# Performance work log

Hardware: AMD Instinct MI355X
Metric: run time of the kernel (lower is better)

## Reference

```python
import jax, jax.numpy as jnp
import numpy as np

B, C, H, W = 8, 256, 64, 64
CQK = C // 8  # query/key channels = 32


def setup_inputs() -> dict:
    key = jax.random.key(0)
    ks = jax.random.split(key, 9)
    s_in = 1.0 / np.sqrt(C)  # conv2d default init scale (kernel_size=1)
    x = jax.random.normal(ks[0], (B, C, H, W), dtype=jnp.float32)
    Wq = jax.random.uniform(ks[1], (CQK, C), jnp.float32, -s_in, s_in)
    bq = jax.random.uniform(ks[2], (CQK,), jnp.float32, -s_in, s_in)
    Wk = jax.random.uniform(ks[3], (CQK, C), jnp.float32, -s_in, s_in)
    bk = jax.random.uniform(ks[4], (CQK,), jnp.float32, -s_in, s_in)
    Wv = jax.random.uniform(ks[5], (C, C), jnp.float32, -s_in, s_in)
    bv = jax.random.uniform(ks[6], (C,), jnp.float32, -s_in, s_in)
    Wf = jax.random.uniform(ks[7], (C, C), jnp.float32, -s_in, s_in)
    bf = jax.random.uniform(ks[8], (C,), jnp.float32, -s_in, s_in)
    return {"x": x, "Wq": Wq, "bq": bq, "Wk": Wk, "bk": bk,
            "Wv": Wv, "bv": bv, "Wf": Wf, "bf": bf}


def reference(x, Wq, bq, Wk, bk, Wv, bv, Wf, bf):
    b, c, h, w = x.shape
    n = h * w
    xf = x.reshape(b, c, n)  # [B, C, N]  (1x1 conv == channel matmul)
    q = jnp.einsum('oc,bcn->bon', Wq, xf) + bq[None, :, None]  # [B, C/8, N]
    k = jnp.einsum('oc,bcn->bon', Wk, xf) + bk[None, :, None]  # [B, C/8, N]
    v = jnp.einsum('oc,bcn->bon', Wv, xf) + bv[None, :, None]  # [B, C, N]
    # energy[b,i,j] = sum_c q[b,c,i] * k[b,c,j]; no scaling (matches source)
    energy = jnp.einsum('bci,bcj->bij', q, k)  # [B, N, N]
    attn = jax.nn.softmax(energy, axis=-1)
    # out[b,c,i] = sum_j v[b,c,j] * attn[b,i,j]
    out = jnp.einsum('bcj,bij->bci', v, attn)  # [B, C, N]
    out = jnp.einsum('oc,bcn->bon', Wf, out) + bf[None, :, None]
    return out.reshape(b, c, h, w)
```

## Files before the change

### kernel.cpp

```cpp
#include <hip/hip_runtime.h>
#include <hip/hip_bf16.h>

#define BATCH 8
#define CCH   256
#define NPOS  4096
#define CQK   32

typedef __attribute__((ext_vector_type(8))) short short8;
typedef __attribute__((ext_vector_type(4))) float f32x4;

__device__ inline unsigned short f2b(float f) {
    __hip_bfloat16 h = __float2bfloat16(f);
    return *reinterpret_cast<unsigned short*>(&h);
}

__device__ inline size_t qk_addr(int b, int n, int c) {
    return ((((size_t)b * 256 + (n >> 4)) * 4 + (c >> 3)) * 16 + (n & 15)) * 8 + (c & 7);
}
__device__ inline size_t v_addr(int b, int c, int j) {
    return (((((size_t)b * 128 + (j >> 5)) * 16 + (c >> 4)) * 4 + ((j >> 3) & 3)) * 16 + (c & 15)) * 8 + (j & 7);
}
__device__ inline size_t wsw_addr(int og, int c, int ol) {
    return ((size_t)(og * 8 + (c >> 5))) * 512 + (((c >> 3) & 3) * 16 + ol) * 8 + (c & 7);
}

__global__ __launch_bounds__(256, 4)
void prep_w_kernel(const float* __restrict__ Wq, const float* __restrict__ Wk,
                   const float* __restrict__ Wv, const float* __restrict__ Wf,
                   unsigned short* __restrict__ wsw)
{
    const int og = blockIdx.x;
    const int t  = threadIdx.x;
    const float* src; int orow;
    if (og < 2)       { src = Wq; orow = og * 16; }
    else if (og < 4)  { src = Wk; orow = (og - 2) * 16; }
    else if (og < 20) { src = Wv; orow = (og - 4) * 16; }
    else              { src = Wf; orow = (og - 20) * 16; }
    #pragma unroll
    for (int e = 0; e < 16; ++e) {
        int idx = t + e * 256;
        int ol = idx >> 8, c = idx & 255;
        wsw[wsw_addr(og, c, ol)] = f2b(src[(orow + ol) * 256 + c]);
    }
}

__global__ __launch_bounds__(256, 2)
void qkv_kernel(const float* __restrict__ x,
                const unsigned short* __restrict__ wsw,
                const float* __restrict__ bq, const float* __restrict__ bk,
                const float* __restrict__ bv,
                unsigned short* __restrict__ qb, unsigned short* __restrict__ kb,
                unsigned short* __restrict__ vb)
{
    __shared__ __align__(16) unsigned short xfrag[4][8][512];

    const int nt   = blockIdx.x;
    const int b    = blockIdx.y;
    const int t    = threadIdx.x;
    const int w    = t >> 6;
    const int lane = t & 63;
    const int q    = lane >> 4;
    const int ln   = lane & 15;
    const int lofs = (q * 16 + ln) * 8;

    {
        const float* xb = x + ((size_t)b * 256) * 4096 + (nt * 64 + w * 16 + ln);
        #pragma unroll
        for (int kk = 0; kk < 8; ++kk) {
            short8 s;
            #pragma unroll
            for (int j = 0; j < 8; ++j)
                ((unsigned short*)&s)[j] = f2b(xb[(size_t)(kk * 32 + q * 8 + j) * 4096]);
            *(short8*)&xfrag[w][kk][lane * 8] = s;
        }
    }
    __syncthreads();

    short8 wqk[8];
    #pragma unroll
    for (int kk = 0; kk < 8; ++kk)
        wqk[kk] = *(const short8*)(wsw + (size_t)(w * 8 + kk) * 512 + lofs);
    const float* bias = (w < 2) ? bq : bk;
    const int cb16 = (w & 1) * 16;
    const float b0 = bias[cb16 + q * 4 + 0];
    const float b1 = bias[cb16 + q * 4 + 1];
    const float b2 = bias[cb16 + q * 4 + 2];
    const float b3 = bias[cb16 + q * 4 + 3];
    unsigned short* dst = (w < 2) ? qb : kb;

    #pragma unroll
    for (int it = 0; it < 4; ++it) {
        short8 xf[8];
        #pragma unroll
        for (int kk = 0; kk < 8; ++kk)
            xf[kk] = *(const short8*)&xfrag[it][kk][lane * 8];

        {
            f32x4 acc = {b0, b1, b2, b3};
            #pragma unroll
            for (int kk = 0; kk < 8; ++kk)
                acc = __builtin_amdgcn_mfma_f32_16x16x32_bf16(wqk[kk], xf[kk], acc, 0, 0, 0);
            ushort4 s = {f2b(acc[0]), f2b(acc[1]), f2b(acc[2]), f2b(acc[3])};
            *(ushort4*)(dst + qk_addr(b, nt * 64 + it * 16 + ln, cb16 + q * 4)) = s;
        }

        #pragma unroll
        for (int oq = 0; oq < 4; ++oq) {
            const int c  = w * 64 + oq * 16 + ln;
            const float bb = bv[c];
            f32x4 acc = {bb, bb, bb, bb};
            const int og = 4 + w * 4 + oq;
            #pragma unroll
            for (int kk = 0; kk < 8; ++kk) {
                short8 bfr = *(const short8*)(wsw + (size_t)(og * 8 + kk) * 512 + lofs);
                acc = __builtin_amdgcn_mfma_f32_16x16x32_bf16(xf[kk], bfr, acc, 0, 0, 0);
            }
            ushort4 s = {f2b(acc[0]), f2b(acc[1]), f2b(acc[2]), f2b(acc[3])};
            *(ushort4*)(vb + v_addr(b, c, nt * 64 + it * 16 + q * 4)) = s;
        }
    }
}

__global__ __launch_bounds__(256, 2)
void attn_kernel(const unsigned short* __restrict__ qb,
                 const unsigned short* __restrict__ kb,
                 const unsigned short* __restrict__ vb,
                 const unsigned short* __restrict__ wsw,
                 const float* __restrict__ bfb, float* __restrict__ out)
{
    __shared__ __align__(16) unsigned short shbuf[64 * 264];
    __shared__ float lred[64];

    const int bid  = blockIdx.x;
    const int b    = bid & 7;
    const int i0   = (bid >> 3) * 64;
    const int t    = threadIdx.x;
    const int w    = t >> 6;
    const int lane = t & 63;
    const int quad = lane >> 4;
    const int ln   = lane & 15;

    const int ibase = i0 + w * 16;
    const int lofs  = (quad * 16 + ln) * 8;

    const short8 qfrag = *(const short8*)(qb + (((size_t)b * 256 + (ibase >> 4)) * 512) + lofs);

    f32x4 acc[4][4];
    #pragma unroll
    for (int it = 0; it < 4; ++it)
        #pragma unroll
        for (int cc = 0; cc < 4; ++cc) acc[it][cc] = (f32x4){0.f, 0.f, 0.f, 0.f};
    float accl[4] = {0.f, 0.f, 0.f, 0.f};

    const unsigned short* kbase = kb + (size_t)b * 256 * 512;
    const unsigned short* vbase = vb + (size_t)b * 128 * 8192;

    short8 kf[4], vf[4][2];
    #pragma unroll
    for (int jc = 0; jc < 4; ++jc)
        kf[jc] = *(const short8*)(kbase + (size_t)jc * 512 + lofs);
    #pragma unroll
    for (int cc = 0; cc < 4; ++cc) {
        vf[cc][0] = *(const short8*)(vbase + (w * 4 + cc) * 512 + lofs);
        vf[cc][1] = *(const short8*)(vbase + 8192 + (w * 4 + cc) * 512 + lofs);
    }

    int pb = 0;
    for (int j0 = 0; j0 < 4096; j0 += 64, pb ^= 1) {
        const int jn = (j0 + 64) & 4095;
        short8 kf_n[4], vf_n[4][2];
        #pragma unroll
        for (int jc = 0; jc < 4; ++jc)
            kf_n[jc] = *(const short8*)(kbase + ((size_t)((jn >> 4) + jc) * 512) + lofs);
        const unsigned short* vt_n = vbase + (size_t)(jn >> 5) * 8192;
        #pragma unroll
        for (int cc = 0; cc < 4; ++cc) {
            vf_n[cc][0] = *(const short8*)(vt_n + (w * 4 + cc) * 512 + lofs);
            vf_n[cc][1] = *(const short8*)(vt_n + 8192 + (w * 4 + cc) * 512 + lofs);
        }
        f32x4 s[4];
        #pragma unroll
        for (int jc = 0; jc < 4; ++jc)
            s[jc] = __builtin_amdgcn_mfma_f32_16x16x32_bf16(qfrag, kf[jc],
                     (f32x4){0.f, 0.f, 0.f, 0.f}, 0, 0, 0);
        #pragma unroll
        for (int jc = 0; jc < 4; ++jc) {
            #pragma unroll
            for (int r = 0; r < 4; ++r) {
                float p = __expf(s[jc][r]);
                accl[r] += p;
                shbuf[((size_t)(pb * 64 + w * 16 + quad * 4 + r)) * 72 + jc * 16 + ln] = f2b(p);
            }
        }
        __syncthreads();
        #pragma unroll
        for (int it = 0; it < 4; ++it) {
            const short8 pf0 = *(const short8*)&shbuf[((size_t)(pb * 64 + it * 16 + ln)) * 72 + quad * 8];
            const short8 pf1 = *(const short8*)&shbuf[((size_t)(pb * 64 + it * 16 + ln)) * 72 + 32 + quad * 8];
            #pragma unroll
            for (int cc = 0; cc < 4; ++cc) {
                acc[it][cc] = __builtin_amdgcn_mfma_f32_16x16x32_bf16(pf0, vf[cc][0], acc[it][cc], 0, 0, 0);
                acc[it][cc] = __builtin_amdgcn_mfma_f32_16x16x32_bf16(pf1, vf[cc][1], acc[it][cc], 0, 0, 0);
            }
        }
        #pragma unroll
        for (int jc = 0; jc < 4; ++jc) kf[jc] = kf_n[jc];
        #pragma unroll
        for (int cc = 0; cc < 4; ++cc) {
            vf[cc][0] = vf_n[cc][0];
            vf[cc][1] = vf_n[cc][1];
        }
    }

    #pragma unroll
    for (int r = 0; r < 4; ++r) {
        float v = accl[r];
        v += __shfl_xor(v, 1, 16);
        v += __shfl_xor(v, 2, 16);
        v += __shfl_xor(v, 4, 16);
        v += __shfl_xor(v, 8, 16);
        if (ln == 0) lred[w * 16 + quad * 4 + r] = v;
    }
    __syncthreads();

    #pragma unroll
    for (int it = 0; it < 4; ++it) {
        float linv[4];
        #pragma unroll
        for (int r = 0; r < 4; ++r) linv[r] = 1.f / lred[it * 16 + quad * 4 + r];
        #pragma unroll
        for (int cc = 0; cc < 4; ++cc) {
            const int c = w * 64 + cc * 16 + ln;
            #pragma unroll
            for (int r = 0; r < 4; ++r)
                shbuf[((size_t)(it * 16 + quad * 4 + r)) * 264 + c] = f2b(acc[it][cc][r] * linv[r]);
        }
    }
    __syncthreads();

    #pragma unroll
    for (int it = 0; it < 4; ++it) {
        short8 af[8];
        #pragma unroll
        for (int kk = 0; kk < 8; ++kk)
            af[kk] = *(const short8*)&shbuf[((size_t)(it * 16 + ln)) * 264 + kk * 32 + quad * 8];
        #pragma unroll
        for (int oq = 0; oq < 4; ++oq) {
            const int o  = w * 64 + oq * 16 + ln;
            const int og = 20 + w * 4 + oq;
            f32x4 pa = {0.f, 0.f, 0.f, 0.f};
            #pragma unroll
            for (int kk = 0; kk < 8; ++kk) {
                short8 bfr = *(const short8*)(wsw + (size_t)(og * 8 + kk) * 512 + lofs);
                pa = __builtin_amdgcn_mfma_f32_16x16x32_bf16(af[kk], bfr, pa, 0, 0, 0);
            }
            const float bias = bfb[o];
            float4 s = {pa[0] + bias, pa[1] + bias, pa[2] + bias, pa[3] + bias};
            *(float4*)(out + (size_t)(b * 256 + o) * 4096 + i0 + it * 16 + quad * 4) = s;
        }
    }
}

extern "C" void kernel_launch(void* const* d_in, const int* in_sizes, int n_in,
                              void* d_out, int out_size, void* d_ws, size_t ws_size,
                              hipStream_t stream)
{
    const float* x  = (const float*)d_in[0];
    const float* Wq = (const float*)d_in[1];
    const float* bq = (const float*)d_in[2];
    const float* Wk = (const float*)d_in[3];
    const float* bk = (const float*)d_in[4];
    const float* Wv = (const float*)d_in[5];
    const float* bv = (const float*)d_in[6];
    const float* Wf = (const float*)d_in[7];
    const float* bf = (const float*)d_in[8];
    float* out = (float*)d_out;

    unsigned short* qb  = (unsigned short*)d_ws;
    unsigned short* kb  = qb + (size_t)BATCH * NPOS * CQK;
    unsigned short* vb  = kb + (size_t)BATCH * NPOS * CQK;
    unsigned short* wsw = vb + (size_t)BATCH * CCH * NPOS;

    prep_w_kernel<<<36, 256, 0, stream>>>(Wq, Wk, Wv, Wf, wsw);
    qkv_kernel<<<dim3(64, 8), 256, 0, stream>>>(x, wsw, bq, bk, bv, qb, kb, vb);
    attn_kernel<<<512, 256, 0, stream>>>(qb, kb, vb, wsw, bf, out);
}
```

Before: 210.3 us.

## Coalesce x loads in QKV, widen to 512 threads, transpose score MFMA with swizzled LDS

The QKV kernel now reads x with float4 loads along the position axis into a padded row-major LDS tile. It runs 512 threads, so two groups of four waves each cover half of the position sub-tiles. The attention kernel swaps the MFMA operands so each lane holds four consecutive key scores for one query row. It writes them as a single 8-byte XOR-swizzled LDS store and reduces the row sum with two cross-quad shuffles instead of four per-row shuffle chains. These changes target uncoalesced strided global loads, scalar LDS stores, bank conflicts and shuffle overhead, at the cost of more LDS per QKV block and more complex addressing.

```diff
diff --git a/kernel.cpp b/kernel.cpp
--- a/kernel.cpp
+++ b/kernel.cpp
@@ -44,7 +44,7 @@
     }
 }
 
-__global__ __launch_bounds__(256, 2)
+__global__ __launch_bounds__(512, 2)
 void qkv_kernel(const float* __restrict__ x,
                 const unsigned short* __restrict__ wsw,
                 const float* __restrict__ bq, const float* __restrict__ bk,
@@ -52,7 +52,7 @@
                 unsigned short* __restrict__ qb, unsigned short* __restrict__ kb,
                 unsigned short* __restrict__ vb)
 {
-    __shared__ __align__(16) unsigned short xfrag[4][8][512];
+    __shared__ __align__(16) unsigned short xl[64 * 280];
 
     const int nt   = blockIdx.x;
     const int b    = blockIdx.y;
@@ -62,16 +62,21 @@
     const int q    = lane >> 4;
     const int ln   = lane & 15;
     const int lofs = (q * 16 + ln) * 8;
+    const int wq   = w & 3;
+    const int ith  = w >> 2;
 
     {
-        const float* xb = x + ((size_t)b * 256) * 4096 + (nt * 64 + w * 16 + ln);
-        #pragma unroll
-        for (int kk = 0; kk < 8; ++kk) {
-            short8 s;
-            #pragma unroll
-            for (int j = 0; j < 8; ++j)
-                ((unsigned short*)&s)[j] = f2b(xb[(size_t)(kk * 32 + q * 8 + j) * 4096]);
-            *(short8*)&xfrag[w][kk][lane * 8] = s;
+        const int c  = t & 255;
+        const int nb = (t >> 8) * 4;
+        const float* xb = x + ((size_t)(b * 256 + c)) * 4096 + nt * 64;
+        #pragma unroll
+        for (int e = 0; e < 8; ++e) {
+            const int n = nb + e * 8;
+            float4 v = *(const float4*)(xb + n);
+            xl[(n + 0) * 280 + c] = f2b(v.x);
+            xl[(n + 1) * 280 + c] = f2b(v.y);
+            xl[(n + 2) * 280 + c] = f2b(v.z);
+            xl[(n + 3) * 280 + c] = f2b(v.w);
         }
     }
     __syncthreads();
@@ -79,21 +84,22 @@
     short8 wqk[8];
     #pragma unroll
     for (int kk = 0; kk < 8; ++kk)
-        wqk[kk] = *(const short8*)(wsw + (size_t)(w * 8 + kk) * 512 + lofs);
-    const float* bias = (w < 2) ? bq : bk;
-    const int cb16 = (w & 1) * 16;
+        wqk[kk] = *(const short8*)(wsw + (size_t)(wq * 8 + kk) * 512 + lofs);
+    const float* bias = (wq < 2) ? bq : bk;
+    const int cb16 = (wq & 1) * 16;
     const float b0 = bias[cb16 + q * 4 + 0];
     const float b1 = bias[cb16 + q * 4 + 1];
     const float b2 = bias[cb16 + q * 4 + 2];
     const float b3 = bias[cb16 + q * 4 + 3];
-    unsigned short* dst = (w < 2) ? qb : kb;
-
-    #pragma unroll
-    for (int it = 0; it < 4; ++it) {
+    unsigned short* dst = (wq < 2) ? qb : kb;
+
+    #pragma unroll
+    for (int itl = 0; itl < 2; ++itl) {
+        const int it = ith * 2 + itl;
         short8 xf[8];
         #pragma unroll
         for (int kk = 0; kk < 8; ++kk)
-            xf[kk] = *(const short8*)&xfrag[it][kk][lane * 8];
+            xf[kk] = *(const short8*)&xl[(it * 16 + ln) * 280 + kk * 32 + q * 8];
 
         {
             f32x4 acc = {b0, b1, b2, b3};
@@ -106,10 +112,10 @@
 
         #pragma unroll
         for (int oq = 0; oq < 4; ++oq) {
-            const int c  = w * 64 + oq * 16 + ln;
+            const int c  = wq * 64 + oq * 16 + ln;
             const float bb = bv[c];
             f32x4 acc = {bb, bb, bb, bb};
-            const int og = 4 + w * 4 + oq;
+            const int og = 4 + wq * 4 + oq;
             #pragma unroll
             for (int kk = 0; kk < 8; ++kk) {
                 short8 bfr = *(const short8*)(wsw + (size_t)(og * 8 + kk) * 512 + lofs);
@@ -142,6 +148,7 @@
 
     const int ibase = i0 + w * 16;
     const int lofs  = (quad * 16 + ln) * 8;
+    const unsigned pswz = (unsigned)((ln & 7) << 4);
 
     const short8 qfrag = *(const short8*)(qb + (((size_t)b * 256 + (ibase >> 4)) * 512) + lofs);
 
@@ -150,7 +157,7 @@
     for (int it = 0; it < 4; ++it)
         #pragma unroll
         for (int cc = 0; cc < 4; ++cc) acc[it][cc] = (f32x4){0.f, 0.f, 0.f, 0.f};
-    float accl[4] = {0.f, 0.f, 0.f, 0.f};
+    float accl = 0.f;
 
     const unsigned short* kbase = kb + (size_t)b * 256 * 512;
     const unsigned short* vbase = vb + (size_t)b * 128 * 8192;
@@ -178,25 +185,31 @@
             vf_n[cc][0] = *(const short8*)(vt_n + (w * 4 + cc) * 512 + lofs);
             vf_n[cc][1] = *(const short8*)(vt_n + 8192 + (w * 4 + cc) * 512 + lofs);
         }
-        f32x4 s[4];
+        f32x4 st[4];
         #pragma unroll
         for (int jc = 0; jc < 4; ++jc)
-            s[jc] = __builtin_amdgcn_mfma_f32_16x16x32_bf16(qfrag, kf[jc],
-                     (f32x4){0.f, 0.f, 0.f, 0.f}, 0, 0, 0);
+            st[jc] = __builtin_amdgcn_mfma_f32_16x16x32_bf16(kf[jc], qfrag,
+                      (f32x4){0.f, 0.f, 0.f, 0.f}, 0, 0, 0);
         #pragma unroll
         for (int jc = 0; jc < 4; ++jc) {
-            #pragma unroll
-            for (int r = 0; r < 4; ++r) {
-                float p = __expf(s[jc][r]);
-                accl[r] += p;
-                shbuf[((size_t)(pb * 64 + w * 16 + quad * 4 + r)) * 72 + jc * 16 + ln] = f2b(p);
-            }
+            float p0 = __expf(st[jc][0]);
+            float p1 = __expf(st[jc][1]);
+            float p2 = __expf(st[jc][2]);
+            float p3 = __expf(st[jc][3]);
+            accl += (p0 + p1) + (p2 + p3);
+            ushort4 pk = {f2b(p0), f2b(p1), f2b(p2), f2b(p3)};
+            unsigned byt = (((unsigned)(pb * 64 + w * 16 + ln)) << 7)
+                         + ((jc * 32 + quad * 8) ^ pswz);
+            *(ushort4*)((unsigned char*)shbuf + byt) = pk;
         }
         __syncthreads();
         #pragma unroll
         for (int it = 0; it < 4; ++it) {
-            const short8 pf0 = *(const short8*)&shbuf[((size_t)(pb * 64 + it * 16 + ln)) * 72 + quad * 8];
-            const short8 pf1 = *(const short8*)&shbuf[((size_t)(pb * 64 + it * 16 + ln)) * 72 + 32 + quad * 8];
+            const unsigned rowb = ((unsigned)(pb * 64 + it * 16 + ln)) << 7;
+            const short8 pf0 = *(const short8*)((const unsigned char*)shbuf
+                                 + rowb + ((quad * 16) ^ pswz));
+            const short8 pf1 = *(const short8*)((const unsigned char*)shbuf
+                                 + rowb + ((64 + quad * 16) ^ pswz));
             #pragma unroll
             for (int cc = 0; cc < 4; ++cc) {
                 acc[it][cc] = __builtin_amdgcn_mfma_f32_16x16x32_bf16(pf0, vf[cc][0], acc[it][cc], 0, 0, 0);
@@ -212,14 +225,11 @@
         }
     }
 
-    #pragma unroll
-    for (int r = 0; r < 4; ++r) {
-        float v = accl[r];
-        v += __shfl_xor(v, 1, 16);
-        v += __shfl_xor(v, 2, 16);
-        v += __shfl_xor(v, 4, 16);
-        v += __shfl_xor(v, 8, 16);
-        if (ln == 0) lred[w * 16 + quad * 4 + r] = v;
+    {
+        float v = accl;
+        v += __shfl_xor(v, 16, 64);
+        v += __shfl_xor(v, 32, 64);
+        if (lane < 16) lred[w * 16 + lane] = v;
     }
     __syncthreads();
 
@@ -282,6 +292,6 @@
     unsigned short* wsw = vb + (size_t)BATCH * CCH * NPOS;
 
     prep_w_kernel<<<36, 256, 0, stream>>>(Wq, Wk, Wv, Wf, wsw);
-    qkv_kernel<<<dim3(64, 8), 256, 0, stream>>>(x, wsw, bq, bk, bv, qb, kb, vb);
+    qkv_kernel<<<dim3(64, 8), 512, 0, stream>>>(x, wsw, bq, bk, bv, qb, kb, vb);
     attn_kernel<<<512, 256, 0, stream>>>(qb, kb, vb, wsw, bf, out);
 }
```

Result: faster. 203.9 us (-3.1%).
